# Kernel tuning notes

Measured on AMD Instinct MI355X. Metric: run time of the kernel, lower is better.

## Reference

```python
import jax, jax.numpy as jnp
import numpy as np

N = 50000
E = 640000
F_IN = 128
F_OUT = 128


def setup_inputs() -> dict:
    key = jax.random.key(0)
    k1, k2, k3, k4, k5 = jax.random.split(key, 5)
    x = jax.random.normal(k1, (N, F_IN), dtype=jnp.float32)
    edge_index = jax.random.randint(k2, (2, E), 0, N, dtype=jnp.int64)
    s = 1.0 / np.sqrt(F_IN)
    W_l = jax.random.uniform(k3, (F_IN, F_OUT), minval=-s, maxval=s, dtype=jnp.float32)
    W_r = jax.random.uniform(k4, (F_IN, F_OUT), minval=-s, maxval=s, dtype=jnp.float32)
    b = jax.random.uniform(k5, (F_OUT,), minval=-s, maxval=s, dtype=jnp.float32)
    return {"x": x, "edge_index": edge_index, "W_l": W_l, "W_r": W_r, "b": b}


def reference(x, edge_index, W_l, W_r, b):
    src, dst = edge_index[0], edge_index[1]
    # gather source-node features along edges: [E, F_in]
    msgs = x[src]
    # mean aggregation at destination nodes
    summed = jax.ops.segment_sum(msgs, dst, num_segments=N)          # [N, F_in]
    counts = jax.ops.segment_sum(jnp.ones((E,), jnp.float32), dst, num_segments=N)
    mean_nb = summed / jnp.maximum(counts, 1.0)[:, None]
    # SAGEConv: lin_l(aggregated) + lin_r(self), bias on lin_l only
    out = mean_nb @ W_l + x @ W_r + b
    return jax.nn.relu(out)
```

## Files before the change

kernel.cpp:

```cpp
#include <hip/hip_runtime.h>

#define N_NODES 50000
#define E_EDGES 640000
#define F 128

typedef __attribute__((ext_vector_type(8))) short short8;
typedef __attribute__((ext_vector_type(4))) float f32x4;

#define DEG_OFF 0
#define OFF_OFF 200704
#define CUR_OFF 401408
#define BSUM_OFF 601600
#define BPRE_OFF 602624
#define WF_OFF 603648
#define SRC_OFF 734720
#define XBF_OFF 3294720
#define MBF_OFF 16094720
#define WS_NEED_FULL 28894720ULL

__device__ __forceinline__ unsigned short f2bf(float f) {
    unsigned int u = __builtin_bit_cast(unsigned int, f);
    u += 0x7FFFu + ((u >> 16) & 1u);
    return (unsigned short)(u >> 16);
}
__device__ __forceinline__ float bfhi2f(unsigned int hi16) {
    return __builtin_bit_cast(float, hi16 & 0xFFFF0000u);
}

__global__ __launch_bounds__(256) void gnn_hist(const int* __restrict__ ei,
                                                int* __restrict__ deg) {
    const int i = blockIdx.x * blockDim.x + threadIdx.x;
    const int stride = gridDim.x * blockDim.x;
    for (int e = i; e < E_EDGES; e += stride)
        atomicAdd(&deg[ei[E_EDGES + e]], 1);
}

__global__ __launch_bounds__(256) void gnn_scan_a(const int* __restrict__ deg,
                                                  int* __restrict__ off,
                                                  int* __restrict__ bsum) {
    __shared__ int s[256];
    const int t = threadIdx.x;
    const int i = blockIdx.x * 256 + t;
    const int v = (i < N_NODES) ? deg[i] : 0;
    s[t] = v;
    __syncthreads();
    for (int d = 1; d < 256; d <<= 1) {
        const int u = (t >= d) ? s[t - d] : 0;
        __syncthreads();
        s[t] += u;
        __syncthreads();
    }
    if (i < N_NODES) off[i] = s[t] - v;
    if (t == 255) bsum[blockIdx.x] = s[255];
}

__global__ __launch_bounds__(256) void gnn_scan_b(const int* __restrict__ bsum,
                                                  int* __restrict__ bpre,
                                                  int* __restrict__ off) {
    __shared__ int s[256];
    const int t = threadIdx.x;
    const int v = (t < 196) ? bsum[t] : 0;
    s[t] = v;
    __syncthreads();
    for (int d = 1; d < 256; d <<= 1) {
        const int u = (t >= d) ? s[t - d] : 0;
        __syncthreads();
        s[t] += u;
        __syncthreads();
    }
    if (t < 196) bpre[t] = s[t] - v;
    if (t == 255) off[N_NODES] = s[255];
}

__global__ __launch_bounds__(256) void gnn_scan_c(const int* __restrict__ bpre,
                                                  int* __restrict__ off,
                                                  int* __restrict__ cur) {
    const int i = blockIdx.x * 256 + threadIdx.x;
    if (i < N_NODES) {
        const int o = off[i] + bpre[blockIdx.x];
        off[i] = o;
        cur[i] = o;
    }
}

__global__ __launch_bounds__(256) void gnn_fill(const int* __restrict__ ei,
                                                int* __restrict__ cur,
                                                int* __restrict__ srcs) {
    const int i = blockIdx.x * blockDim.x + threadIdx.x;
    const int stride = gridDim.x * blockDim.x;
    for (int e = i; e < E_EDGES; e += stride) {
        const int d = ei[E_EDGES + e];
        const int p = atomicAdd(&cur[d], 1);
        srcs[p] = ei[e];
    }
}

__global__ __launch_bounds__(256) void gnn_wprep(const float* __restrict__ Wl,
                                                 const float* __restrict__ Wr,
                                                 short* __restrict__ Wf) {
    const int tid = blockIdx.x * 256 + threadIdx.x;
    const int lane = tid & 63;
    const int frag = tid >> 6;
    const int kstep = frag >> 3;
    const int ct = frag & 7;
    const int kb = kstep * 32 + (lane >> 4) * 8;
    const int c = ct * 16 + (lane & 15);
    short8 v;
#pragma unroll
    for (int j = 0; j < 8; ++j) {
        const int k = kb + j;
        const float f = (k < F) ? Wl[k * F + c] : Wr[(k - F) * F + c];
        v[j] = (short)f2bf(f);
    }
    *reinterpret_cast<short8*>(Wf + (size_t)tid * 8) = v;
}

__global__ __launch_bounds__(256) void gnn_xcast(const float* __restrict__ x,
                                                 unsigned short* __restrict__ xbf) {
    const size_t i = ((size_t)blockIdx.x * 256 + threadIdx.x) * 8;
    if (i >= (size_t)N_NODES * F) return;
    const float4 a0 = *reinterpret_cast<const float4*>(x + i);
    const float4 a1 = *reinterpret_cast<const float4*>(x + i + 4);
    short8 v;
    v[0] = (short)f2bf(a0.x); v[1] = (short)f2bf(a0.y);
    v[2] = (short)f2bf(a0.z); v[3] = (short)f2bf(a0.w);
    v[4] = (short)f2bf(a1.x); v[5] = (short)f2bf(a1.y);
    v[6] = (short)f2bf(a1.z); v[7] = (short)f2bf(a1.w);
    *reinterpret_cast<short8*>((short*)xbf + i) = v;
}

__global__ __launch_bounds__(256) void gnn_aggregate_bf(
    const unsigned short* __restrict__ xbf, const int* __restrict__ off,
    const int* __restrict__ srcs, unsigned short* __restrict__ mbf) {
    const int node = blockIdx.x * 4 + (threadIdx.x >> 6);
    if (node >= N_NODES) return;
    const int lane = threadIdx.x & 63;
    const int half = lane >> 5;
    const int l32 = lane & 31;
    const int o0 = off[node];
    const int o1 = off[node + 1];
    const unsigned short* xb = xbf + (size_t)l32 * 4;
    f32x4 acc0 = {0.f, 0.f, 0.f, 0.f}, acc1 = {0.f, 0.f, 0.f, 0.f};
    f32x4 acc2 = {0.f, 0.f, 0.f, 0.f}, acc3 = {0.f, 0.f, 0.f, 0.f};
    int j = o0;
    for (; j + 8 <= o1; j += 8) {
        const uint2 a = *reinterpret_cast<const uint2*>(xb + (size_t)srcs[j + half] * F);
        const uint2 b = *reinterpret_cast<const uint2*>(xb + (size_t)srcs[j + 2 + half] * F);
        const uint2 c = *reinterpret_cast<const uint2*>(xb + (size_t)srcs[j + 4 + half] * F);
        const uint2 d = *reinterpret_cast<const uint2*>(xb + (size_t)srcs[j + 6 + half] * F);
        acc0[0] += bfhi2f(a.x << 16); acc0[1] += bfhi2f(a.x);
        acc0[2] += bfhi2f(a.y << 16); acc0[3] += bfhi2f(a.y);
        acc1[0] += bfhi2f(b.x << 16); acc1[1] += bfhi2f(b.x);
        acc1[2] += bfhi2f(b.y << 16); acc1[3] += bfhi2f(b.y);
        acc2[0] += bfhi2f(c.x << 16); acc2[1] += bfhi2f(c.x);
        acc2[2] += bfhi2f(c.y << 16); acc2[3] += bfhi2f(c.y);
        acc3[0] += bfhi2f(d.x << 16); acc3[1] += bfhi2f(d.x);
        acc3[2] += bfhi2f(d.y << 16); acc3[3] += bfhi2f(d.y);
    }
    for (; j + 4 <= o1; j += 4) {
        const uint2 a = *reinterpret_cast<const uint2*>(xb + (size_t)srcs[j + half] * F);
        const uint2 b = *reinterpret_cast<const uint2*>(xb + (size_t)srcs[j + 2 + half] * F);
        acc0[0] += bfhi2f(a.x << 16); acc0[1] += bfhi2f(a.x);
        acc0[2] += bfhi2f(a.y << 16); acc0[3] += bfhi2f(a.y);
        acc1[0] += bfhi2f(b.x << 16); acc1[1] += bfhi2f(b.x);
        acc1[2] += bfhi2f(b.y << 16); acc1[3] += bfhi2f(b.y);
    }
    for (; j < o1; j += 2) {
        const int jj = j + half;
        const uint2 a = *reinterpret_cast<const uint2*>(
            xb + (size_t)srcs[(jj < o1) ? jj : o0] * F);
        if (jj < o1) {
            acc0[0] += bfhi2f(a.x << 16); acc0[1] += bfhi2f(a.x);
            acc0[2] += bfhi2f(a.y << 16); acc0[3] += bfhi2f(a.y);
        }
    }
    acc0 += acc1 + acc2 + acc3;
    f32x4 o;
    o[0] = __shfl_xor(acc0[0], 32, 64);
    o[1] = __shfl_xor(acc0[1], 32, 64);
    o[2] = __shfl_xor(acc0[2], 32, 64);
    o[3] = __shfl_xor(acc0[3], 32, 64);
    acc0 += o;
    if (half == 0) {
        const float inv = 1.0f / (float)max(o1 - o0, 1);
        acc0 *= inv;
        ushort4 m;
        m.x = f2bf(acc0[0]); m.y = f2bf(acc0[1]);
        m.z = f2bf(acc0[2]); m.w = f2bf(acc0[3]);
        *reinterpret_cast<ushort4*>(mbf + (size_t)node * F + l32 * 4) = m;
    }
}

__global__ __launch_bounds__(256) void gnn_finalize_bf(
    const unsigned short* __restrict__ xbf, const unsigned short* __restrict__ mbf,
    const short* __restrict__ Wf, const float* __restrict__ bias,
    float* __restrict__ out) {
    const int t = threadIdx.x;
    const int lane = t & 63;
    const int wv = t >> 6;
    const int r0 = blockIdx.x * 64 + wv * 16;
    const int rl = lane & 15;
    const int kg = lane >> 4;
    const int arow = r0 + rl;
    const int arow_c = (arow < N_NODES) ? arow : (N_NODES - 1);

    f32x4 acc[8];
#pragma unroll
    for (int ct = 0; ct < 8; ++ct) acc[ct] = (f32x4){0.f, 0.f, 0.f, 0.f};

#pragma unroll
    for (int kstep = 0; kstep < 8; ++kstep) {
        const int k0 = kstep * 32 + kg * 8;
        const unsigned short* asrc =
            (kstep < 4) ? (mbf + (size_t)arow_c * F + k0)
                        : (xbf + (size_t)arow_c * F + (k0 - F));
        const short8 af = *reinterpret_cast<const short8*>(asrc);
#pragma unroll
        for (int ct = 0; ct < 8; ++ct) {
            const short8 bf = *reinterpret_cast<const short8*>(
                Wf + (size_t)((kstep * 8 + ct) * 64 + lane) * 8);
            acc[ct] = __builtin_amdgcn_mfma_f32_16x16x32_bf16(af, bf, acc[ct],
                                                              0, 0, 0);
        }
    }

#pragma unroll
    for (int ct = 0; ct < 8; ++ct) {
        const int c = ct * 16 + rl;
        const float bv = bias[c];
#pragma unroll
        for (int r = 0; r < 4; ++r) {
            const int row = r0 + kg * 4 + r;
            if (row < N_NODES)
                out[(size_t)row * F + c] = fmaxf(acc[ct][r] + bv, 0.0f);
        }
    }
}

__global__ __launch_bounds__(256) void gnn_aggregate(
    const float* __restrict__ x, const int* __restrict__ off,
    const int* __restrict__ srcs, float* __restrict__ out) {
    const int node = blockIdx.x * 4 + (threadIdx.x >> 6);
    if (node >= N_NODES) return;
    const int lane = threadIdx.x & 63;
    const int half = lane >> 5;
    const int l32 = lane & 31;
    const int o0 = off[node];
    const int o1 = off[node + 1];
    f32x4 acc0 = {0.f, 0.f, 0.f, 0.f};
    f32x4 acc1 = {0.f, 0.f, 0.f, 0.f};
    int j = o0;
    for (; j + 4 <= o1; j += 4) {
        const int sA = srcs[j + half];
        const int sB = srcs[j + 2 + half];
        acc0 += *reinterpret_cast<const f32x4*>(x + (size_t)sA * F + l32 * 4);
        acc1 += *reinterpret_cast<const f32x4*>(x + (size_t)sB * F + l32 * 4);
    }
    for (; j < o1; j += 2) {
        const int jj = j + half;
        const int s = srcs[(jj < o1) ? jj : o0];
        f32x4 v = *reinterpret_cast<const f32x4*>(x + (size_t)s * F + l32 * 4);
        if (jj >= o1) v = (f32x4){0.f, 0.f, 0.f, 0.f};
        acc0 += v;
    }
    acc0 += acc1;
    f32x4 o;
    o[0] = __shfl_xor(acc0[0], 32, 64);
    o[1] = __shfl_xor(acc0[1], 32, 64);
    o[2] = __shfl_xor(acc0[2], 32, 64);
    o[3] = __shfl_xor(acc0[3], 32, 64);
    acc0 += o;
    if (half == 0) {
        const float inv = 1.0f / (float)max(o1 - o0, 1);
        acc0 *= inv;
        *reinterpret_cast<f32x4*>(out + (size_t)node * F + l32 * 4) = acc0;
    }
}

__global__ __launch_bounds__(256) void gnn_finalize_mfma(
    const float* __restrict__ x, const short* __restrict__ Wf,
    const float* __restrict__ bias, float* __restrict__ out) {
    const int t = threadIdx.x;
    const int lane = t & 63;
    const int wv = t >> 6;
    const int r0 = blockIdx.x * 64 + wv * 16;
    const int rl = lane & 15;
    const int kg = lane >> 4;
    const int arow = r0 + rl;
    const int arow_c = (arow < N_NODES) ? arow : (N_NODES - 1);
    f32x4 acc[8];
#pragma unroll
    for (int ct = 0; ct < 8; ++ct) acc[ct] = (f32x4){0.f, 0.f, 0.f, 0.f};
#pragma unroll
    for (int kstep = 0; kstep < 8; ++kstep) {
        const int k0 = kstep * 32 + kg * 8;
        const float* asrc = (kstep < 4) ? (out + (size_t)arow_c * F + k0)
                                        : (x + (size_t)arow_c * F + (k0 - F));
        const float4 a0 = *reinterpret_cast<const float4*>(asrc);
        const float4 a1 = *reinterpret_cast<const float4*>(asrc + 4);
        short8 af;
        af[0] = (short)f2bf(a0.x); af[1] = (short)f2bf(a0.y);
        af[2] = (short)f2bf(a0.z); af[3] = (short)f2bf(a0.w);
        af[4] = (short)f2bf(a1.x); af[5] = (short)f2bf(a1.y);
        af[6] = (short)f2bf(a1.z); af[7] = (short)f2bf(a1.w);
#pragma unroll
        for (int ct = 0; ct < 8; ++ct) {
            const short8 bf = *reinterpret_cast<const short8*>(
                Wf + (size_t)((kstep * 8 + ct) * 64 + lane) * 8);
            acc[ct] = __builtin_amdgcn_mfma_f32_16x16x32_bf16(af, bf, acc[ct],
                                                              0, 0, 0);
        }
    }
#pragma unroll
    for (int ct = 0; ct < 8; ++ct) {
        const int c = ct * 16 + rl;
        const float bv = bias[c];
#pragma unroll
        for (int r = 0; r < 4; ++r) {
            const int row = r0 + kg * 4 + r;
            if (row < N_NODES)
                out[(size_t)row * F + c] = fmaxf(acc[ct][r] + bv, 0.0f);
        }
    }
}

extern "C" void kernel_launch(void* const* d_in, const int* in_sizes, int n_in,
                              void* d_out, int out_size, void* d_ws,
                              size_t ws_size, hipStream_t stream) {
    const float* x = (const float*)d_in[0];
    const int* ei = (const int*)d_in[1];
    const float* Wl = (const float*)d_in[2];
    const float* Wr = (const float*)d_in[3];
    const float* b = (const float*)d_in[4];
    float* out = (float*)d_out;

    char* ws = (char*)d_ws;
    int* deg = (int*)(ws + DEG_OFF);
    int* off = (int*)(ws + OFF_OFF);
    int* cur = (int*)(ws + CUR_OFF);
    int* bsum = (int*)(ws + BSUM_OFF);
    int* bpre = (int*)(ws + BPRE_OFF);
    short* Wf = (short*)(ws + WF_OFF);
    int* srcs = (int*)(ws + SRC_OFF);
    unsigned short* xbf = (unsigned short*)(ws + XBF_OFF);
    unsigned short* mbf = (unsigned short*)(ws + MBF_OFF);

    hipMemsetAsync(deg, 0, N_NODES * sizeof(int), stream);

    gnn_hist<<<2048, 256, 0, stream>>>(ei, deg);
    gnn_scan_a<<<196, 256, 0, stream>>>(deg, off, bsum);
    gnn_scan_b<<<1, 256, 0, stream>>>(bsum, bpre, off);
    gnn_scan_c<<<196, 256, 0, stream>>>(bpre, off, cur);
    gnn_fill<<<2048, 256, 0, stream>>>(ei, cur, srcs);
    gnn_wprep<<<16, 256, 0, stream>>>(Wl, Wr, Wf);

    if (ws_size >= WS_NEED_FULL) {
        gnn_xcast<<<((N_NODES * F / 8) + 255) / 256, 256, 0, stream>>>(x, xbf);
        gnn_aggregate_bf<<<(N_NODES + 3) / 4, 256, 0, stream>>>(xbf, off, srcs,
                                                                mbf);
        gnn_finalize_bf<<<(N_NODES + 63) / 64, 256, 0, stream>>>(xbf, mbf, Wf,
                                                                 b, out);
    } else {
        gnn_aggregate<<<(N_NODES + 3) / 4, 256, 0, stream>>>(x, off, srcs, out);
        gnn_finalize_mfma<<<(N_NODES + 63) / 64, 256, 0, stream>>>(x, Wf, b,
                                                                   out);
    }
}
```

Before: 202.1 us.

## Fuse aggregation with MFMA finalize via LDS and merge prep/scan kernels

Each 64-node block now aggregates neighbor means into a swizzled shared-memory tile and feeds that tile straight into the bf16 MFMA linear layer. This removes the global mean buffer write and read-back and one launch. The x cast, weight prep and degree histogram are also merged into one multi-role kernel, and the two scan-fixup kernels are merged by having each block recompute the small block-sum scan. The cost is lower parallelism in aggregation: 16 nodes per wave run serially, with only 782 blocks, which may hurt latency hiding on the irregular gathers.

```diff
diff --git a/kernel.cpp b/kernel.cpp
--- a/kernel.cpp
+++ b/kernel.cpp
@@ -15,8 +15,12 @@
 #define WF_OFF 603648
 #define SRC_OFF 734720
 #define XBF_OFF 3294720
-#define MBF_OFF 16094720
-#define WS_NEED_FULL 28894720ULL
+#define WS_NEED_FULL 16094720ULL
+
+#define XCAST_BLKS 3125
+#define WPREP_BLKS 16
+#define HIST_BLKS 2048
+#define PREP_GRID (XCAST_BLKS + WPREP_BLKS + HIST_BLKS)
 
 __device__ __forceinline__ unsigned short f2bf(float f) {
     unsigned int u = __builtin_bit_cast(unsigned int, f);
@@ -27,12 +31,46 @@
     return __builtin_bit_cast(float, hi16 & 0xFFFF0000u);
 }
 
-__global__ __launch_bounds__(256) void gnn_hist(const int* __restrict__ ei,
-                                                int* __restrict__ deg) {
-    const int i = blockIdx.x * blockDim.x + threadIdx.x;
-    const int stride = gridDim.x * blockDim.x;
-    for (int e = i; e < E_EDGES; e += stride)
-        atomicAdd(&deg[ei[E_EDGES + e]], 1);
+__global__ __launch_bounds__(256) void gnn_prep(
+    const float* __restrict__ x, const int* __restrict__ ei,
+    const float* __restrict__ Wl, const float* __restrict__ Wr,
+    short* __restrict__ Wf, unsigned short* __restrict__ xbf,
+    int* __restrict__ deg, int full) {
+    const int bid = blockIdx.x;
+    const int t = threadIdx.x;
+    if (bid < XCAST_BLKS) {
+        if (!full) return;
+        const size_t i = ((size_t)bid * 256 + t) * 8;
+        const float4 a0 = *reinterpret_cast<const float4*>(x + i);
+        const float4 a1 = *reinterpret_cast<const float4*>(x + i + 4);
+        short8 v;
+        v[0] = (short)f2bf(a0.x); v[1] = (short)f2bf(a0.y);
+        v[2] = (short)f2bf(a0.z); v[3] = (short)f2bf(a0.w);
+        v[4] = (short)f2bf(a1.x); v[5] = (short)f2bf(a1.y);
+        v[6] = (short)f2bf(a1.z); v[7] = (short)f2bf(a1.w);
+        *reinterpret_cast<short8*>((short*)xbf + i) = v;
+    } else if (bid < XCAST_BLKS + WPREP_BLKS) {
+        const int tid = (bid - XCAST_BLKS) * 256 + t;
+        const int lane = tid & 63;
+        const int frag = tid >> 6;
+        const int kstep = frag >> 3;
+        const int ct = frag & 7;
+        const int kb = kstep * 32 + (lane >> 4) * 8;
+        const int c = ct * 16 + (lane & 15);
+        short8 v;
+#pragma unroll
+        for (int j = 0; j < 8; ++j) {
+            const int k = kb + j;
+            const float f = (k < F) ? Wl[k * F + c] : Wr[(k - F) * F + c];
+            v[j] = (short)f2bf(f);
+        }
+        *reinterpret_cast<short8*>(Wf + (size_t)tid * 8) = v;
+    } else {
+        const int i = (bid - XCAST_BLKS - WPREP_BLKS) * 256 + t;
+        const int stride = HIST_BLKS * 256;
+        for (int e = i; e < E_EDGES; e += stride)
+            atomicAdd(&deg[ei[E_EDGES + e]], 1);
+    }
 }
 
 __global__ __launch_bounds__(256) void gnn_scan_a(const int* __restrict__ deg,
@@ -54,13 +92,13 @@
     if (t == 255) bsum[blockIdx.x] = s[255];
 }
 
-__global__ __launch_bounds__(256) void gnn_scan_b(const int* __restrict__ bsum,
-                                                  int* __restrict__ bpre,
-                                                  int* __restrict__ off) {
+__global__ __launch_bounds__(256) void gnn_scan2(const int* __restrict__ bsum,
+                                                 int* __restrict__ off,
+                                                 int* __restrict__ cur) {
     __shared__ int s[256];
     const int t = threadIdx.x;
-    const int v = (t < 196) ? bsum[t] : 0;
-    s[t] = v;
+    const int bid = blockIdx.x;
+    s[t] = (t < 196) ? bsum[t] : 0;
     __syncthreads();
     for (int d = 1; d < 256; d <<= 1) {
         const int u = (t >= d) ? s[t - d] : 0;
@@ -68,19 +106,14 @@
         s[t] += u;
         __syncthreads();
     }
-    if (t < 196) bpre[t] = s[t] - v;
-    if (t == 255) off[N_NODES] = s[255];
-}
-
-__global__ __launch_bounds__(256) void gnn_scan_c(const int* __restrict__ bpre,
-                                                  int* __restrict__ off,
-                                                  int* __restrict__ cur) {
-    const int i = blockIdx.x * 256 + threadIdx.x;
+    const int myPre = (bid == 0) ? 0 : s[bid - 1];
+    const int i = bid * 256 + t;
     if (i < N_NODES) {
-        const int o = off[i] + bpre[blockIdx.x];
+        const int o = off[i] + myPre;
         off[i] = o;
         cur[i] = o;
     }
+    if (bid == 0 && t == 0) off[N_NODES] = s[195];
 }
 
 __global__ __launch_bounds__(256) void gnn_fill(const int* __restrict__ ei,
@@ -95,114 +128,84 @@
     }
 }
 
-__global__ __launch_bounds__(256) void gnn_wprep(const float* __restrict__ Wl,
-                                                 const float* __restrict__ Wr,
-                                                 short* __restrict__ Wf) {
-    const int tid = blockIdx.x * 256 + threadIdx.x;
-    const int lane = tid & 63;
-    const int frag = tid >> 6;
-    const int kstep = frag >> 3;
-    const int ct = frag & 7;
-    const int kb = kstep * 32 + (lane >> 4) * 8;
-    const int c = ct * 16 + (lane & 15);
-    short8 v;
-#pragma unroll
-    for (int j = 0; j < 8; ++j) {
-        const int k = kb + j;
-        const float f = (k < F) ? Wl[k * F + c] : Wr[(k - F) * F + c];
-        v[j] = (short)f2bf(f);
-    }
-    *reinterpret_cast<short8*>(Wf + (size_t)tid * 8) = v;
-}
-
-__global__ __launch_bounds__(256) void gnn_xcast(const float* __restrict__ x,
-                                                 unsigned short* __restrict__ xbf) {
-    const size_t i = ((size_t)blockIdx.x * 256 + threadIdx.x) * 8;
-    if (i >= (size_t)N_NODES * F) return;
-    const float4 a0 = *reinterpret_cast<const float4*>(x + i);
-    const float4 a1 = *reinterpret_cast<const float4*>(x + i + 4);
-    short8 v;
-    v[0] = (short)f2bf(a0.x); v[1] = (short)f2bf(a0.y);
-    v[2] = (short)f2bf(a0.z); v[3] = (short)f2bf(a0.w);
-    v[4] = (short)f2bf(a1.x); v[5] = (short)f2bf(a1.y);
-    v[6] = (short)f2bf(a1.z); v[7] = (short)f2bf(a1.w);
-    *reinterpret_cast<short8*>((short*)xbf + i) = v;
-}
-
-__global__ __launch_bounds__(256) void gnn_aggregate_bf(
+__global__ __launch_bounds__(256) void gnn_agg_fin(
     const unsigned short* __restrict__ xbf, const int* __restrict__ off,
-    const int* __restrict__ srcs, unsigned short* __restrict__ mbf) {
-    const int node = blockIdx.x * 4 + (threadIdx.x >> 6);
-    if (node >= N_NODES) return;
-    const int lane = threadIdx.x & 63;
+    const int* __restrict__ srcs, const short* __restrict__ Wf,
+    const float* __restrict__ bias, float* __restrict__ out) {
+    __shared__ unsigned short mean_s[64 * 128];
+    const int t = threadIdx.x;
+    const int lane = t & 63;
+    const int wv = t >> 6;
+    const int nb0 = blockIdx.x * 64;
     const int half = lane >> 5;
     const int l32 = lane & 31;
-    const int o0 = off[node];
-    const int o1 = off[node + 1];
-    const unsigned short* xb = xbf + (size_t)l32 * 4;
-    f32x4 acc0 = {0.f, 0.f, 0.f, 0.f}, acc1 = {0.f, 0.f, 0.f, 0.f};
-    f32x4 acc2 = {0.f, 0.f, 0.f, 0.f}, acc3 = {0.f, 0.f, 0.f, 0.f};
-    int j = o0;
-    for (; j + 8 <= o1; j += 8) {
-        const uint2 a = *reinterpret_cast<const uint2*>(xb + (size_t)srcs[j + half] * F);
-        const uint2 b = *reinterpret_cast<const uint2*>(xb + (size_t)srcs[j + 2 + half] * F);
-        const uint2 c = *reinterpret_cast<const uint2*>(xb + (size_t)srcs[j + 4 + half] * F);
-        const uint2 d = *reinterpret_cast<const uint2*>(xb + (size_t)srcs[j + 6 + half] * F);
-        acc0[0] += bfhi2f(a.x << 16); acc0[1] += bfhi2f(a.x);
-        acc0[2] += bfhi2f(a.y << 16); acc0[3] += bfhi2f(a.y);
-        acc1[0] += bfhi2f(b.x << 16); acc1[1] += bfhi2f(b.x);
-        acc1[2] += bfhi2f(b.y << 16); acc1[3] += bfhi2f(b.y);
-        acc2[0] += bfhi2f(c.x << 16); acc2[1] += bfhi2f(c.x);
-        acc2[2] += bfhi2f(c.y << 16); acc2[3] += bfhi2f(c.y);
-        acc3[0] += bfhi2f(d.x << 16); acc3[1] += bfhi2f(d.x);
-        acc3[2] += bfhi2f(d.y << 16); acc3[3] += bfhi2f(d.y);
-    }
-    for (; j + 4 <= o1; j += 4) {
-        const uint2 a = *reinterpret_cast<const uint2*>(xb + (size_t)srcs[j + half] * F);
-        const uint2 b = *reinterpret_cast<const uint2*>(xb + (size_t)srcs[j + 2 + half] * F);
-        acc0[0] += bfhi2f(a.x << 16); acc0[1] += bfhi2f(a.x);
-        acc0[2] += bfhi2f(a.y << 16); acc0[3] += bfhi2f(a.y);
-        acc1[0] += bfhi2f(b.x << 16); acc1[1] += bfhi2f(b.x);
-        acc1[2] += bfhi2f(b.y << 16); acc1[3] += bfhi2f(b.y);
-    }
-    for (; j < o1; j += 2) {
-        const int jj = j + half;
-        const uint2 a = *reinterpret_cast<const uint2*>(
-            xb + (size_t)srcs[(jj < o1) ? jj : o0] * F);
-        if (jj < o1) {
+
+    for (int i = 0; i < 16; ++i) {
+        const int node = nb0 + wv * 16 + i;
+        if (node >= N_NODES) break;
+        const int o0 = off[node];
+        const int o1 = off[node + 1];
+        const unsigned short* xb = xbf + (size_t)l32 * 4;
+        f32x4 acc0 = {0.f, 0.f, 0.f, 0.f}, acc1 = {0.f, 0.f, 0.f, 0.f};
+        f32x4 acc2 = {0.f, 0.f, 0.f, 0.f}, acc3 = {0.f, 0.f, 0.f, 0.f};
+        int j = o0;
+        for (; j + 8 <= o1; j += 8) {
+            const uint2 a = *reinterpret_cast<const uint2*>(xb + (size_t)srcs[j + half] * F);
+            const uint2 b = *reinterpret_cast<const uint2*>(xb + (size_t)srcs[j + 2 + half] * F);
+            const uint2 c = *reinterpret_cast<const uint2*>(xb + (size_t)srcs[j + 4 + half] * F);
+            const uint2 d = *reinterpret_cast<const uint2*>(xb + (size_t)srcs[j + 6 + half] * F);
             acc0[0] += bfhi2f(a.x << 16); acc0[1] += bfhi2f(a.x);
             acc0[2] += bfhi2f(a.y << 16); acc0[3] += bfhi2f(a.y);
-        }
-    }
-    acc0 += acc1 + acc2 + acc3;
-    f32x4 o;
-    o[0] = __shfl_xor(acc0[0], 32, 64);
-    o[1] = __shfl_xor(acc0[1], 32, 64);
-    o[2] = __shfl_xor(acc0[2], 32, 64);
-    o[3] = __shfl_xor(acc0[3], 32, 64);
-    acc0 += o;
-    if (half == 0) {
-        const float inv = 1.0f / (float)max(o1 - o0, 1);
-        acc0 *= inv;
-        ushort4 m;
-        m.x = f2bf(acc0[0]); m.y = f2bf(acc0[1]);
-        m.z = f2bf(acc0[2]); m.w = f2bf(acc0[3]);
-        *reinterpret_cast<ushort4*>(mbf + (size_t)node * F + l32 * 4) = m;
-    }
-}
-
-__global__ __launch_bounds__(256) void gnn_finalize_bf(
-    const unsigned short* __restrict__ xbf, const unsigned short* __restrict__ mbf,
-    const short* __restrict__ Wf, const float* __restrict__ bias,
-    float* __restrict__ out) {
-    const int t = threadIdx.x;
-    const int lane = t & 63;
-    const int wv = t >> 6;
-    const int r0 = blockIdx.x * 64 + wv * 16;
+            acc1[0] += bfhi2f(b.x << 16); acc1[1] += bfhi2f(b.x);
+            acc1[2] += bfhi2f(b.y << 16); acc1[3] += bfhi2f(b.y);
+            acc2[0] += bfhi2f(c.x << 16); acc2[1] += bfhi2f(c.x);
+            acc2[2] += bfhi2f(c.y << 16); acc2[3] += bfhi2f(c.y);
+            acc3[0] += bfhi2f(d.x << 16); acc3[1] += bfhi2f(d.x);
+            acc3[2] += bfhi2f(d.y << 16); acc3[3] += bfhi2f(d.y);
+        }
+        for (; j + 4 <= o1; j += 4) {
+            const uint2 a = *reinterpret_cast<const uint2*>(xb + (size_t)srcs[j + half] * F);
+            const uint2 b = *reinterpret_cast<const uint2*>(xb + (size_t)srcs[j + 2 + half] * F);
+            acc0[0] += bfhi2f(a.x << 16); acc0[1] += bfhi2f(a.x);
+            acc0[2] += bfhi2f(a.y << 16); acc0[3] += bfhi2f(a.y);
+            acc1[0] += bfhi2f(b.x << 16); acc1[1] += bfhi2f(b.x);
+            acc1[2] += bfhi2f(b.y << 16); acc1[3] += bfhi2f(b.y);
+        }
+        for (; j < o1; j += 2) {
+            const int jj = j + half;
+            const uint2 a = *reinterpret_cast<const uint2*>(
+                xb + (size_t)srcs[(jj < o1) ? jj : o0] * F);
+            if (jj < o1) {
+                acc0[0] += bfhi2f(a.x << 16); acc0[1] += bfhi2f(a.x);
+                acc0[2] += bfhi2f(a.y << 16); acc0[3] += bfhi2f(a.y);
+            }
+        }
+        acc0 += acc1 + acc2 + acc3;
+        f32x4 o;
+        o[0] = __shfl_xor(acc0[0], 32, 64);
+        o[1] = __shfl_xor(acc0[1], 32, 64);
+        o[2] = __shfl_xor(acc0[2], 32, 64);
+        o[3] = __shfl_xor(acc0[3], 32, 64);
+        acc0 += o;
+        if (half == 0) {
+            const float inv = 1.0f / (float)max(o1 - o0, 1);
+            acc0 *= inv;
+            ushort4 m;
+            m.x = f2bf(acc0[0]); m.y = f2bf(acc0[1]);
+            m.z = f2bf(acc0[2]); m.w = f2bf(acc0[3]);
+            const int r = wv * 16 + i;
+            const int byteoff = r * 256 + ((l32 * 8) ^ ((r & 7) << 4));
+            *reinterpret_cast<ushort4*>((char*)mean_s + byteoff) = m;
+        }
+    }
+    __syncthreads();
+
     const int rl = lane & 15;
     const int kg = lane >> 4;
+    const int r0 = nb0 + wv * 16;
     const int arow = r0 + rl;
     const int arow_c = (arow < N_NODES) ? arow : (N_NODES - 1);
+    const int rr = arow_c - nb0;
 
     f32x4 acc[8];
 #pragma unroll
@@ -210,11 +213,15 @@
 
 #pragma unroll
     for (int kstep = 0; kstep < 8; ++kstep) {
-        const int k0 = kstep * 32 + kg * 8;
-        const unsigned short* asrc =
-            (kstep < 4) ? (mbf + (size_t)arow_c * F + k0)
-                        : (xbf + (size_t)arow_c * F + (k0 - F));
-        const short8 af = *reinterpret_cast<const short8*>(asrc);
+        short8 af;
+        if (kstep < 4) {
+            const int cb = (kstep * 64 + kg * 16) ^ ((rr & 7) << 4);
+            af = *reinterpret_cast<const short8*>((const char*)mean_s +
+                                                  rr * 256 + cb);
+        } else {
+            const int k0 = kstep * 32 + kg * 8 - F;
+            af = *reinterpret_cast<const short8*>(xbf + (size_t)arow_c * F + k0);
+        }
 #pragma unroll
         for (int ct = 0; ct < 8; ++ct) {
             const short8 bf = *reinterpret_cast<const short8*>(
@@ -339,27 +346,21 @@
     int* off = (int*)(ws + OFF_OFF);
     int* cur = (int*)(ws + CUR_OFF);
     int* bsum = (int*)(ws + BSUM_OFF);
-    int* bpre = (int*)(ws + BPRE_OFF);
     short* Wf = (short*)(ws + WF_OFF);
     int* srcs = (int*)(ws + SRC_OFF);
     unsigned short* xbf = (unsigned short*)(ws + XBF_OFF);
-    unsigned short* mbf = (unsigned short*)(ws + MBF_OFF);
+
+    const int full = (ws_size >= WS_NEED_FULL) ? 1 : 0;
 
     hipMemsetAsync(deg, 0, N_NODES * sizeof(int), stream);
-
-    gnn_hist<<<2048, 256, 0, stream>>>(ei, deg);
+    gnn_prep<<<PREP_GRID, 256, 0, stream>>>(x, ei, Wl, Wr, Wf, xbf, deg, full);
     gnn_scan_a<<<196, 256, 0, stream>>>(deg, off, bsum);
-    gnn_scan_b<<<1, 256, 0, stream>>>(bsum, bpre, off);
-    gnn_scan_c<<<196, 256, 0, stream>>>(bpre, off, cur);
+    gnn_scan2<<<196, 256, 0, stream>>>(bsum, off, cur);
     gnn_fill<<<2048, 256, 0, stream>>>(ei, cur, srcs);
-    gnn_wprep<<<16, 256, 0, stream>>>(Wl, Wr, Wf);
-
-    if (ws_size >= WS_NEED_FULL) {
-        gnn_xcast<<<((N_NODES * F / 8) + 255) / 256, 256, 0, stream>>>(x, xbf);
-        gnn_aggregate_bf<<<(N_NODES + 3) / 4, 256, 0, stream>>>(xbf, off, srcs,
-                                                                mbf);
-        gnn_finalize_bf<<<(N_NODES + 63) / 64, 256, 0, stream>>>(xbf, mbf, Wf,
-                                                                 b, out);
+
+    if (full) {
+        gnn_agg_fin<<<(N_NODES + 63) / 64, 256, 0, stream>>>(xbf, off, srcs,
+                                                             Wf, b, out);
     } else {
         gnn_aggregate<<<(N_NODES + 3) / 4, 256, 0, stream>>>(x, off, srcs, out);
         gnn_finalize_mfma<<<(N_NODES + 63) / 64, 256, 0, stream>>>(x, Wf, b,
```

New measurement: 207.2 us. 1.03x slower.
